# Kernel optimization log

Measured on AMD Instinct MI355X. Metric: run time of the kernel, lower is better.

The kernel has to match this reference:

```python
import jax, jax.numpy as jnp
import numpy as np

N, E, F, H, O = 50000, 800000, 64, 128, 64
GRID_SIZE, SPLINE_ORDER = 3, 2


def make_grid(in_features, grid_size=GRID_SIZE, spline_order=SPLINE_ORDER, grid_range=(-1.0, 1.0)):
    h = (grid_range[1] - grid_range[0]) / grid_size
    pts = jnp.arange(-spline_order, grid_size + spline_order + 1, dtype=jnp.float32) * h + grid_range[0]
    return jnp.tile(pts[None, :], (in_features, 1))  # [in, grid_size + 2*order + 1]


def b_splines(x, grid, spline_order=SPLINE_ORDER):
    # x: [B, in], grid: [in, G+2k+1] -> bases [B, in, G+k]
    xe = x[..., None]
    bases = ((xe >= grid[:, :-1]) & (xe < grid[:, 1:])).astype(x.dtype)
    for k in range(1, spline_order + 1):
        bases = ((xe - grid[:, : -(k + 1)]) / (grid[:, k:-1] - grid[:, : -(k + 1)]) * bases[..., :-1]
                 + (grid[:, k + 1:] - xe) / (grid[:, k + 1:] - grid[:, 1:-k]) * bases[..., 1:])
    return bases


def setup_inputs() -> dict:
    key = jax.random.key(0)
    ks = jax.random.split(key, 12)
    x = jax.random.normal(ks[0], (N, F), dtype=jnp.float32)
    contexts = jax.random.normal(ks[1], (E, F), dtype=jnp.float32)
    attn = jax.random.uniform(ks[2], (E,), dtype=jnp.float32)
    seg_ids = jnp.sort(jax.random.randint(ks[3], (E,), 0, N, dtype=jnp.int32))
    s = 0.05
    Wn = jax.random.normal(ks[4], (H, F), dtype=jnp.float32) * s
    bn = jnp.zeros((H,), dtype=jnp.float32)
    Wc = jax.random.normal(ks[5], (H, F), dtype=jnp.float32) * s
    bc = jnp.zeros((H,), dtype=jnp.float32)
    Wu = jax.random.normal(ks[6], (O, H), dtype=jnp.float32) * s
    bu = jnp.zeros((O,), dtype=jnp.float32)
    n_coef = GRID_SIZE + SPLINE_ORDER
    base_w = jax.random.normal(ks[7], (O, O), dtype=jnp.float32) * s
    spline_w = jax.random.normal(ks[8], (O, O, n_coef), dtype=jnp.float32) * s
    spline_scaler = jnp.ones((O, O), dtype=jnp.float32)
    grid = make_grid(O)
    return dict(x=x, contexts=contexts, attn=attn, seg_ids=seg_ids, Wn=Wn, bn=bn,
                Wc=Wc, bc=bc, Wu=Wu, bu=bu, base_w=base_w, spline_w=spline_w,
                spline_scaler=spline_scaler, grid=grid)


def reference(x, contexts, attn, seg_ids, Wn, bn, Wc, bc, Wu, bu, base_w, spline_w, spline_scaler, grid):
    n = x.shape[0]
    # per-edge context transform, attention weighting
    ctx_t = contexts @ Wc.T + bc                      # [E, H]
    weighted = ctx_t * attn[:, None]                  # [E, H]
    seg_sum = jax.ops.segment_sum(weighted, seg_ids, num_segments=n)        # [N, H]
    deg = jax.ops.segment_sum(jnp.ones_like(attn), seg_ids, num_segments=n)  # [N]
    ctx_agg = seg_sum / jnp.maximum(deg, 1.0)[:, None]  # mean over edges per node
    x_t = x @ Wn.T + bn                               # [N, H]
    upd = (x_t + ctx_agg) @ Wu.T + bu                 # [N, O]
    # KANLinear (efficient-kan): silu base path + b-spline path
    base_out = jax.nn.silu(upd) @ base_w.T            # [N, O]
    bases = b_splines(upd, grid)                      # [N, O, G+k]
    scaled_sw = spline_w * spline_scaler[..., None]   # [O, O, G+k]
    spline_out = jnp.einsum('bik,oik->bo', bases, scaled_sw)
    kan_out = base_out + spline_out
    # nodes with no contexts keep their raw features (num_features == output_dim)
    return jnp.where(deg[:, None] > 0, kan_out, x)
```

## Files before the change

### kernel.cpp

```cpp
#include <hip/hip_runtime.h>
#include <hip/hip_bf16.h>

#define NN 50000
#define NE 800000

typedef short short8 __attribute__((ext_vector_type(8)));
typedef float f32x4 __attribute__((ext_vector_type(4)));
typedef unsigned short ushort_t;

static __device__ __forceinline__ unsigned bits(float f) { return __float_as_uint(f); }
static __device__ __forceinline__ float hi_f(float v) {
  return __uint_as_float(bits(v) & 0xFFFF0000u);
}
static __device__ __forceinline__ ushort_t hi_u(float v) { return (ushort_t)(bits(v) >> 16); }
static __device__ __forceinline__ unsigned pack_hi(float v0, float v1) {
  return (bits(v0) >> 16) | (bits(v1) & 0xFFFF0000u);
}
static __device__ __forceinline__ unsigned pack_lo(float v0, float v1) {
  float l0 = v0 - hi_f(v0), l1 = v1 - hi_f(v1);
  return (bits(l0) >> 16) | (bits(l1) & 0xFFFF0000u);
}

#define MFMA(a, b, c) __builtin_amdgcn_mfma_f32_16x16x32_bf16(a, b, c, 0, 0, 0)

__global__ __launch_bounds__(256) void kA_pack_off(
    const float* __restrict__ Wn, const float* __restrict__ Wc,
    const float* __restrict__ Wu, const float* __restrict__ base_w,
    const float* __restrict__ spline_w, const float* __restrict__ scaler,
    const int* __restrict__ seg,
    ushort_t* __restrict__ p1h, ushort_t* __restrict__ p2h,
    ushort_t* __restrict__ p3h, int* __restrict__ off) {
  int t = blockIdx.x * 256 + threadIdx.x;
  if (t < 4096) {
    int l = t & 63, lm = l & 15, lk = l >> 4;
    if (t < 2048) {
      int nt = t >> 8, ks = (t >> 6) & 3;
      int h = nt * 16 + lm;
#pragma unroll
      for (int j = 0; j < 8; ++j) {
        int f = ks * 32 + lk * 8 + j;
        float v = (f < 64) ? Wn[h * 64 + f] : Wc[h * 64 + (f - 64)];
        p1h[t * 8 + j] = hi_u(v);
      }
    }
    if (t < 1024) {
      int nt = t >> 8, ks = (t >> 6) & 3;
      int o = nt * 16 + lm;
#pragma unroll
      for (int j = 0; j < 8; ++j) {
        int hh = ks * 32 + lk * 8 + j;
        p2h[t * 8 + j] = hi_u(Wu[o * 128 + hh]);
      }
    }
    if (t < 3072) {
      int nt = t / 768, ks = (t >> 6) % 12;
      int o = nt * 16 + lm;
#pragma unroll
      for (int j = 0; j < 8; ++j) {
        int k = ks * 32 + lk * 8 + j;
        int i = k / 6, c = k % 6;
        float v = (c == 0) ? base_w[o * 64 + i]
                           : spline_w[(o * 64 + i) * 5 + (c - 1)] * scaler[o * 64 + i];
        p3h[t * 8 + j] = hi_u(v);
      }
    }
  }
  int e = t;
  if (e < NE) {
    int s1 = seg[e];
    if (e == 0) {
      for (int n = 0; n <= s1; ++n) off[n] = 0;
    } else {
      int s0 = seg[e - 1];
      for (int n = s0 + 1; n <= s1; ++n) off[n] = e;
    }
    if (e == NE - 1) {
      for (int n = s1 + 1; n <= NN; ++n) off[n] = NE;
    }
  }
}

__global__ __launch_bounds__(512, 4) void k1234(
    const float* __restrict__ x,
    const float* __restrict__ contexts, const float* __restrict__ attn,
    const int* __restrict__ off,
    const float* __restrict__ bn, const float* __restrict__ bc,
    const float* __restrict__ bu,
    const ushort_t* __restrict__ p1h, const ushort_t* __restrict__ p2h,
    const ushort_t* __restrict__ p3h,
    const float* __restrict__ gridp, float* __restrict__ out) {
  __shared__ __align__(16) unsigned char arena[49152];
  __shared__ float ap[64], degl[64];
  ushort_t* Uh = (ushort_t*)arena;
  ushort_t* Ul = (ushort_t*)(arena + 16384);
  ushort_t* Th = (ushort_t*)(arena + 32768);
  ushort_t* Vh = (ushort_t*)arena;

  int tid = threadIdx.x;
  int n0 = blockIdx.x * 64;
  int w = tid >> 6, l = tid & 63;
  int wm = w >> 2, wn = w & 3;
  int lm = l & 15, lk = l >> 4;
  const short8* P1h = (const short8*)p1h;
  const short8* P2h = (const short8*)p2h;
  const short8* P3h = (const short8*)p3h;

  {
    const float4* x4 = (const float4*)x;
    int row = tid >> 3, slot = tid & 7;
    int n = n0 + row;
    float4 a = make_float4(0.f, 0.f, 0.f, 0.f), b = a;
    if (n < NN) {
      a = x4[(size_t)n * 16 + slot * 2];
      b = x4[(size_t)n * 16 + slot * 2 + 1];
    }
    uint4 hp, lp;
    hp.x = pack_hi(a.x, a.y); hp.y = pack_hi(a.z, a.w);
    hp.z = pack_hi(b.x, b.y); hp.w = pack_hi(b.z, b.w);
    lp.x = pack_lo(a.x, a.y); lp.y = pack_lo(a.z, a.w);
    lp.z = pack_lo(b.x, b.y); lp.w = pack_lo(b.z, b.w);
    int idx = (row * 128 + slot * 8) ^ ((row & 7) << 3);
    *(uint4*)&Uh[idx] = hp;
    *(uint4*)&Ul[idx] = lp;
  }

  {
    int nb = n0 + w * 8;
    int offv = 0;
    if (l < 9) offv = off[min(nb + l, NN)];
    int sub = l >> 4, fq = l & 15;
    const float4* ctx4 = (const float4*)contexts;
#pragma unroll 1
    for (int i = 0; i < 8; ++i) {
      int s = __shfl(offv, i);
      int e_end = __shfl(offv, i + 1);
      int deg_i = e_end - s;
      float4 S = make_float4(0.f, 0.f, 0.f, 0.f);
      float A = 0.f;
      if (deg_i > 0) {
        int last = e_end - 1;
        for (int e0 = s; e0 < e_end; e0 += 16) {
          float a[4];
          float4 c[4];
#pragma unroll
          for (int u = 0; u < 4; ++u) {
            int eu = e0 + 4 * u + sub;
            a[u] = (eu < e_end) ? attn[eu] : 0.f;
            c[u] = ctx4[(size_t)min(eu, last) * 16 + fq];
          }
#pragma unroll
          for (int u = 0; u < 4; ++u) {
            S.x += a[u] * c[u].x;
            S.y += a[u] * c[u].y;
            S.z += a[u] * c[u].z;
            S.w += a[u] * c[u].w;
            A += a[u];
          }
        }
      }
#pragma unroll
      for (int m = 16; m <= 32; m <<= 1) {
        S.x += __shfl_xor(S.x, m);
        S.y += __shfl_xor(S.y, m);
        S.z += __shfl_xor(S.z, m);
        S.w += __shfl_xor(S.w, m);
        A += __shfl_xor(A, m);
      }
      float deg = (float)deg_i;
      float inv = 1.f / fmaxf(deg, 1.f);
      int row = w * 8 + i;
      if (l < 16) {
        float ox = S.x * inv, oy = S.y * inv, oz = S.z * inv, ow = S.w * inv;
        uint2 hp, lp;
        hp.x = pack_hi(ox, oy);
        hp.y = pack_hi(oz, ow);
        lp.x = pack_lo(ox, oy);
        lp.y = pack_lo(oz, ow);
        int idx = (row * 128 + 64 + l * 4) ^ ((row & 7) << 3);
        *(uint2*)&Uh[idx] = hp;
        *(uint2*)&Ul[idx] = lp;
      }
      if (l == 0) { ap[row] = A * inv; degl[row] = deg; }
    }
  }

  short8 B1[2][4], B2[4];
#pragma unroll
  for (int q = 0; q < 2; ++q)
#pragma unroll
    for (int ks = 0; ks < 4; ++ks) B1[q][ks] = P1h[((2 * wn + q) * 4 + ks) * 64 + l];
#pragma unroll
  for (int ks = 0; ks < 4; ++ks) B2[ks] = P2h[(wn * 4 + ks) * 64 + l];

  __syncthreads();

  int swzA = (lm & 7) << 3;

  f32x4 acc1[2][2];
#pragma unroll
  for (int q = 0; q < 2; ++q)
#pragma unroll
    for (int ms = 0; ms < 2; ++ms) acc1[q][ms] = (f32x4){0.f, 0.f, 0.f, 0.f};
#pragma unroll
  for (int ks = 0; ks < 4; ++ks) {
    short8 ah[2], al[2];
#pragma unroll
    for (int ms = 0; ms < 2; ++ms) {
      int ai = (((2 * wm + ms) * 16 + lm) * 128 + ks * 32 + lk * 8) ^ swzA;
      ah[ms] = *(const short8*)&Uh[ai];
      al[ms] = *(const short8*)&Ul[ai];
    }
#pragma unroll
    for (int q = 0; q < 2; ++q)
#pragma unroll
      for (int ms = 0; ms < 2; ++ms) {
        acc1[q][ms] = MFMA(ah[ms], B1[q][ks], acc1[q][ms]);
        acc1[q][ms] = MFMA(al[ms], B1[q][ks], acc1[q][ms]);
      }
  }
#pragma unroll
  for (int q = 0; q < 2; ++q) {
    int h = (2 * wn + q) * 16 + lm;
    float bnv = bn[h], bcv = bc[h];
#pragma unroll
    for (int ms = 0; ms < 2; ++ms) {
#pragma unroll
      for (int r = 0; r < 4; ++r) {
        int node = (2 * wm + ms) * 16 + lk * 4 + r;
        float t = acc1[q][ms][r] + bnv + ap[node] * bcv;
        Th[(node * 128 + h) ^ ((node & 7) << 3)] = hi_u(t);
      }
    }
  }
  __syncthreads();

  short8 B3[12];
#pragma unroll
  for (int ks = 0; ks < 12; ++ks) B3[ks] = P3h[(wn * 12 + ks) * 64 + l];
  float g[8];
#pragma unroll
  for (int j = 0; j < 8; ++j) g[j] = gridp[j];
  float r1[7], r2[6];
#pragma unroll
  for (int j = 0; j < 7; ++j) r1[j] = 1.f / (g[j + 1] - g[j]);
#pragma unroll
  for (int j = 0; j < 6; ++j) r2[j] = 1.f / (g[j + 2] - g[j]);
  float buv = bu[wn * 16 + lm];

  f32x4 acc2[2];
  acc2[0] = (f32x4){0.f, 0.f, 0.f, 0.f};
  acc2[1] = (f32x4){0.f, 0.f, 0.f, 0.f};
#pragma unroll
  for (int ks = 0; ks < 4; ++ks) {
#pragma unroll
    for (int ms = 0; ms < 2; ++ms) {
      int ai = (((2 * wm + ms) * 16 + lm) * 128 + ks * 32 + lk * 8) ^ swzA;
      short8 ah = *(const short8*)&Th[ai];
      acc2[ms] = MFMA(ah, B2[ks], acc2[ms]);
    }
  }

#pragma unroll
  for (int half = 0; half < 2; ++half) {
    if (wm == half) {
#pragma unroll
      for (int ms = 0; ms < 2; ++ms) {
#pragma unroll
        for (int r = 0; r < 4; ++r) {
          float xv = acc2[ms][r] + buv;
          float sil = xv / (1.f + __expf(-xv));
          float b0[7], b1[6], b2[5];
#pragma unroll
          for (int q = 0; q < 7; ++q) b0[q] = (xv >= g[q] && xv < g[q + 1]) ? 1.f : 0.f;
#pragma unroll
          for (int q = 0; q < 6; ++q)
            b1[q] = (xv - g[q]) * r1[q] * b0[q] + (g[q + 2] - xv) * r1[q + 1] * b0[q + 1];
#pragma unroll
          for (int q = 0; q < 5; ++q)
            b2[q] = (xv - g[q]) * r2[q] * b1[q] + (g[q + 3] - xv) * r2[q + 1] * b1[q + 1];
          int ln = ms * 16 + lk * 4 + r;
          int base = ln * 392 + (wn * 16 + lm) * 6;
          *(unsigned*)&Vh[base + 0] = pack_hi(sil, b2[0]);
          *(unsigned*)&Vh[base + 2] = pack_hi(b2[1], b2[2]);
          *(unsigned*)&Vh[base + 4] = pack_hi(b2[3], b2[4]);
        }
      }
    }
    __syncthreads();

    f32x4 accK = (f32x4){0.f, 0.f, 0.f, 0.f};
#pragma unroll
    for (int ks = 0; ks < 12; ++ks) {
      short8 ah = *(const short8*)&Vh[(wm * 16 + lm) * 392 + ks * 32 + lk * 8];
      accK = MFMA(ah, B3[ks], accK);
    }
    if (half == 0) __syncthreads();

    int o = wn * 16 + lm;
#pragma unroll
    for (int r = 0; r < 4; ++r) {
      int node = half * 32 + wm * 16 + lk * 4 + r;
      int n = n0 + node;
      if (n < NN) {
        float val = accK[r];
        if (degl[node] <= 0.f) val = x[(size_t)n * 64 + o];
        out[(size_t)n * 64 + o] = val;
      }
    }
  }
}

extern "C" void kernel_launch(void* const* d_in, const int* in_sizes, int n_in,
                              void* d_out, int out_size, void* d_ws, size_t ws_size,
                              hipStream_t stream) {
  const float* x        = (const float*)d_in[0];
  const float* contexts = (const float*)d_in[1];
  const float* attn     = (const float*)d_in[2];
  const int*   seg      = (const int*)d_in[3];
  const float* Wn       = (const float*)d_in[4];
  const float* bn       = (const float*)d_in[5];
  const float* Wc       = (const float*)d_in[6];
  const float* bc       = (const float*)d_in[7];
  const float* Wu       = (const float*)d_in[8];
  const float* bu       = (const float*)d_in[9];
  const float* base_w   = (const float*)d_in[10];
  const float* spline_w = (const float*)d_in[11];
  const float* scaler   = (const float*)d_in[12];
  const float* gridp    = (const float*)d_in[13];
  float* out = (float*)d_out;

  ushort_t* us  = (ushort_t*)d_ws;
  ushort_t* p1h = us;
  ushort_t* p2h = p1h + 16384;
  ushort_t* p3h = p2h + 8192;
  int*   off    = (int*)(p3h + 24576);

  kA_pack_off<<<3125, 256, 0, stream>>>(Wn, Wc, Wu, base_w, spline_w, scaler, seg,
                                        p1h, p2h, p3h, off);
  k1234<<<782, 512, 0, stream>>>(x, contexts, attn, off, bn, bc, bu,
                                 p1h, p2h, p3h, gridp, out);
}
```

Before: 67.49 us.

## Split edge aggregation into separate kernel with one wave per node

Moves the per-node edge segment aggregation out of the fused GEMM kernel into its own kernel, with one wavefront per node across 12500 blocks, writing bf16 hi/lo split means plus attention mean and degree to workspace. The GEMM/KAN kernel then loads these precomputed values alongside x. The aim is better latency hiding and load balance for the irregular gather over roughly 205 MB of context data, at the cost of an extra launch and a global round trip of about 13 MB of intermediates. Occupancy of the main kernel's launch bounds is lowered from 4 to 3.

```diff
diff --git a/kernel.cpp b/kernel.cpp
--- a/kernel.cpp
+++ b/kernel.cpp
@@ -80,10 +80,72 @@
   }
 }
 
-__global__ __launch_bounds__(512, 4) void k1234(
+__global__ __launch_bounds__(256) void k1_edge_agg(
+    const float* __restrict__ contexts, const float* __restrict__ attn,
+    const int* __restrict__ off, ushort_t* __restrict__ Sph,
+    ushort_t* __restrict__ Spl, float* __restrict__ aprime,
+    float* __restrict__ degw) {
+  int n = blockIdx.x * 4 + (threadIdx.x >> 6);
+  int lane = threadIdx.x & 63;
+  if (n >= NN) return;
+  int s = off[n];
+  int e_end = off[n + 1];
+  int deg_i = e_end - s;
+
+  int sub = lane >> 4;
+  int fq = lane & 15;
+  const float4* ctx4 = (const float4*)contexts;
+
+  float4 S = make_float4(0.f, 0.f, 0.f, 0.f);
+  float A = 0.f;
+  if (deg_i > 0) {
+    int last = e_end - 1;
+    for (int e0 = s; e0 < e_end; e0 += 16) {
+      float a[4];
+      float4 c[4];
+#pragma unroll
+      for (int u = 0; u < 4; ++u) {
+        int eu = e0 + 4 * u + sub;
+        a[u] = (eu < e_end) ? attn[eu] : 0.f;
+        c[u] = ctx4[(size_t)min(eu, last) * 16 + fq];
+      }
+#pragma unroll
+      for (int u = 0; u < 4; ++u) {
+        S.x += a[u] * c[u].x;
+        S.y += a[u] * c[u].y;
+        S.z += a[u] * c[u].z;
+        S.w += a[u] * c[u].w;
+        A += a[u];
+      }
+    }
+  }
+#pragma unroll
+  for (int m = 16; m <= 32; m <<= 1) {
+    S.x += __shfl_xor(S.x, m);
+    S.y += __shfl_xor(S.y, m);
+    S.z += __shfl_xor(S.z, m);
+    S.w += __shfl_xor(S.w, m);
+    A += __shfl_xor(A, m);
+  }
+  float deg = (float)deg_i;
+  float inv = 1.f / fmaxf(deg, 1.f);
+  if (lane < 16) {
+    float ox = S.x * inv, oy = S.y * inv, oz = S.z * inv, ow = S.w * inv;
+    uint2 hp, lp;
+    hp.x = pack_hi(ox, oy);
+    hp.y = pack_hi(oz, ow);
+    lp.x = pack_lo(ox, oy);
+    lp.y = pack_lo(oz, ow);
+    *(uint2*)&Sph[(size_t)n * 64 + lane * 4] = hp;
+    *(uint2*)&Spl[(size_t)n * 64 + lane * 4] = lp;
+  }
+  if (lane == 0) { aprime[n] = A * inv; degw[n] = deg; }
+}
+
+__global__ __launch_bounds__(512, 3) void k234(
     const float* __restrict__ x,
-    const float* __restrict__ contexts, const float* __restrict__ attn,
-    const int* __restrict__ off,
+    const ushort_t* __restrict__ Sph, const ushort_t* __restrict__ Spl,
+    const float* __restrict__ aprime, const float* __restrict__ degw,
     const float* __restrict__ bn, const float* __restrict__ bc,
     const float* __restrict__ bu,
     const ushort_t* __restrict__ p1h, const ushort_t* __restrict__ p2h,
@@ -105,93 +167,52 @@
   const short8* P2h = (const short8*)p2h;
   const short8* P3h = (const short8*)p3h;
 
+  short8 B1[2][4], B2[4];
+#pragma unroll
+  for (int q = 0; q < 2; ++q)
+#pragma unroll
+    for (int ks = 0; ks < 4; ++ks) B1[q][ks] = P1h[((2 * wn + q) * 4 + ks) * 64 + l];
+#pragma unroll
+  for (int ks = 0; ks < 4; ++ks) B2[ks] = P2h[(wn * 4 + ks) * 64 + l];
+
   {
     const float4* x4 = (const float4*)x;
-    int row = tid >> 3, slot = tid & 7;
-    int n = n0 + row;
-    float4 a = make_float4(0.f, 0.f, 0.f, 0.f), b = a;
-    if (n < NN) {
-      a = x4[(size_t)n * 16 + slot * 2];
-      b = x4[(size_t)n * 16 + slot * 2 + 1];
-    }
-    uint4 hp, lp;
-    hp.x = pack_hi(a.x, a.y); hp.y = pack_hi(a.z, a.w);
-    hp.z = pack_hi(b.x, b.y); hp.w = pack_hi(b.z, b.w);
-    lp.x = pack_lo(a.x, a.y); lp.y = pack_lo(a.z, a.w);
-    lp.z = pack_lo(b.x, b.y); lp.w = pack_lo(b.z, b.w);
-    int idx = (row * 128 + slot * 8) ^ ((row & 7) << 3);
-    *(uint4*)&Uh[idx] = hp;
-    *(uint4*)&Ul[idx] = lp;
-  }
-
-  {
-    int nb = n0 + w * 8;
-    int offv = 0;
-    if (l < 9) offv = off[min(nb + l, NN)];
-    int sub = l >> 4, fq = l & 15;
-    const float4* ctx4 = (const float4*)contexts;
-#pragma unroll 1
-    for (int i = 0; i < 8; ++i) {
-      int s = __shfl(offv, i);
-      int e_end = __shfl(offv, i + 1);
-      int deg_i = e_end - s;
-      float4 S = make_float4(0.f, 0.f, 0.f, 0.f);
-      float A = 0.f;
-      if (deg_i > 0) {
-        int last = e_end - 1;
-        for (int e0 = s; e0 < e_end; e0 += 16) {
-          float a[4];
-          float4 c[4];
-#pragma unroll
-          for (int u = 0; u < 4; ++u) {
-            int eu = e0 + 4 * u + sub;
-            a[u] = (eu < e_end) ? attn[eu] : 0.f;
-            c[u] = ctx4[(size_t)min(eu, last) * 16 + fq];
-          }
-#pragma unroll
-          for (int u = 0; u < 4; ++u) {
-            S.x += a[u] * c[u].x;
-            S.y += a[u] * c[u].y;
-            S.z += a[u] * c[u].z;
-            S.w += a[u] * c[u].w;
-            A += a[u];
-          }
+    const uint4* Sh4 = (const uint4*)Sph;
+    const uint4* Sl4 = (const uint4*)Spl;
+#pragma unroll
+    for (int q = tid; q < 1024; q += 512) {
+      int row = q >> 4, slot = q & 15;
+      int n = n0 + row;
+      int idx = (row * 128 + slot * 8) ^ ((row & 7) << 3);
+      if (slot < 8) {
+        float4 a = make_float4(0.f, 0.f, 0.f, 0.f), b = a;
+        if (n < NN) {
+          a = x4[(size_t)n * 16 + slot * 2];
+          b = x4[(size_t)n * 16 + slot * 2 + 1];
         }
-      }
-#pragma unroll
-      for (int m = 16; m <= 32; m <<= 1) {
-        S.x += __shfl_xor(S.x, m);
-        S.y += __shfl_xor(S.y, m);
-        S.z += __shfl_xor(S.z, m);
-        S.w += __shfl_xor(S.w, m);
-        A += __shfl_xor(A, m);
-      }
-      float deg = (float)deg_i;
-      float inv = 1.f / fmaxf(deg, 1.f);
-      int row = w * 8 + i;
-      if (l < 16) {
-        float ox = S.x * inv, oy = S.y * inv, oz = S.z * inv, ow = S.w * inv;
-        uint2 hp, lp;
-        hp.x = pack_hi(ox, oy);
-        hp.y = pack_hi(oz, ow);
-        lp.x = pack_lo(ox, oy);
-        lp.y = pack_lo(oz, ow);
-        int idx = (row * 128 + 64 + l * 4) ^ ((row & 7) << 3);
-        *(uint2*)&Uh[idx] = hp;
-        *(uint2*)&Ul[idx] = lp;
-      }
-      if (l == 0) { ap[row] = A * inv; degl[row] = deg; }
-    }
-  }
-
-  short8 B1[2][4], B2[4];
-#pragma unroll
-  for (int q = 0; q < 2; ++q)
-#pragma unroll
-    for (int ks = 0; ks < 4; ++ks) B1[q][ks] = P1h[((2 * wn + q) * 4 + ks) * 64 + l];
-#pragma unroll
-  for (int ks = 0; ks < 4; ++ks) B2[ks] = P2h[(wn * 4 + ks) * 64 + l];
-
+        uint4 hp, lp;
+        hp.x = pack_hi(a.x, a.y); hp.y = pack_hi(a.z, a.w);
+        hp.z = pack_hi(b.x, b.y); hp.w = pack_hi(b.z, b.w);
+        lp.x = pack_lo(a.x, a.y); lp.y = pack_lo(a.z, a.w);
+        lp.z = pack_lo(b.x, b.y); lp.w = pack_lo(b.z, b.w);
+        *(uint4*)&Uh[idx] = hp;
+        *(uint4*)&Ul[idx] = lp;
+      } else {
+        uint4 vh = make_uint4(0u, 0u, 0u, 0u), vl = vh;
+        if (n < NN) {
+          vh = Sh4[(size_t)n * 8 + (slot & 7)];
+          vl = Sl4[(size_t)n * 8 + (slot & 7)];
+        }
+        *(uint4*)&Uh[idx] = vh;
+        *(uint4*)&Ul[idx] = vl;
+      }
+    }
+  }
+  if (tid < 64) {
+    int n = n0 + tid;
+    ap[tid] = (n < NN) ? aprime[n] : 0.f;
+    degl[tid] = (n < NN) ? degw[n] : 1.f;
+  }
   __syncthreads();
 
   int swzA = (lm & 7) << 3;
@@ -330,13 +351,18 @@
   float* out = (float*)d_out;
 
   ushort_t* us  = (ushort_t*)d_ws;
-  ushort_t* p1h = us;
+  ushort_t* Sph = us;
+  ushort_t* Spl = Sph + 3200000;
+  ushort_t* p1h = Spl + 3200000;
   ushort_t* p2h = p1h + 16384;
   ushort_t* p3h = p2h + 8192;
-  int*   off    = (int*)(p3h + 24576);
+  float* aprime = (float*)(p3h + 24576);
+  float* degw   = aprime + 50000;
+  int*   off    = (int*)(degw + 50000);
 
   kA_pack_off<<<3125, 256, 0, stream>>>(Wn, Wc, Wu, base_w, spline_w, scaler, seg,
                                         p1h, p2h, p3h, off);
-  k1234<<<782, 512, 0, stream>>>(x, contexts, attn, off, bn, bc, bu,
-                                 p1h, p2h, p3h, gridp, out);
-}
+  k1_edge_agg<<<12500, 256, 0, stream>>>(contexts, attn, off, Sph, Spl, aprime, degw);
+  k234<<<782, 512, 0, stream>>>(x, Sph, Spl, aprime, degw, bn, bc, bu,
+                                p1h, p2h, p3h, gridp, out);
+}
```

After: 72.29 us. 7.1% more time.
